# Optimization experiments

Hardware: AMD Instinct MI355X
Metric: run time of the kernel (lower is better)

Reference implementation:

```python
import jax, jax.numpy as jnp
import numpy as np

IN_FEATURES = 1024
OUT_FEATURES = 1024
BATCH = 32768
EPS = 1e-6


def setup_inputs() -> dict:
    key = jax.random.key(0)
    kx, kw = jax.random.split(key)
    x = jax.random.normal(kx, (BATCH, IN_FEATURES), dtype=jnp.float32)
    # xavier-uniform-like init for weight [out, in]
    limit = np.sqrt(6.0 / (IN_FEATURES + OUT_FEATURES)).astype(np.float32)
    W = jax.random.uniform(kw, (OUT_FEATURES, IN_FEATURES), dtype=jnp.float32,
                           minval=-limit, maxval=limit)
    b = jnp.zeros((OUT_FEATURES,), dtype=jnp.float32)
    return {"x": x, "W": W, "b": b}


def reference(x, W, b):
    # sign with sign(0) -> +1
    binary_w = jnp.where(W >= 0, 1.0, -1.0).astype(W.dtype)  # [out, in]
    # per-output-row scale, detached in the original (no grad flows through it)
    scale = jnp.maximum(jnp.mean(jnp.abs(W), axis=1, keepdims=True), EPS)  # [out, 1]
    # F.linear(x, binary_w * scale, b) = x @ (binary_w * scale).T + b
    return jnp.einsum('ni,oi->no', x, binary_w * scale) + b
```

## Files before the change

### kernel.cpp

```cpp
#include <hip/hip_runtime.h>


typedef short short8 __attribute__((ext_vector_type(8)));
typedef float f32x4 __attribute__((ext_vector_type(4)));

#define BATCH 32768
#define IN_F  1024
#define OUT_F 1024
#define EPS   1e-6f

#define BM 128
#define BN 128
#define BK 32

__device__ __forceinline__ ushort f2bf(float f) {
  unsigned u = __builtin_bit_cast(unsigned, f);
  u += 0x7FFFu + ((u >> 16) & 1u);
  return (ushort)(u >> 16);
}

__global__ void bin_kernel(const float* __restrict__ W,
                           ushort* __restrict__ Wb,
                           float* __restrict__ scale) {
  int row = blockIdx.x;
  int t = threadIdx.x;
  const float4* wr = (const float4*)(W + (size_t)row * IN_F);
  ushort4* wb = (ushort4*)(Wb + (size_t)row * IN_F);
  float s = 0.f;
#pragma unroll
  for (int i = 0; i < 4; ++i) {
    float4 v = wr[i * 64 + t];
    ushort4 u;
    u.x = (v.x >= 0.f) ? 0x3F80 : 0xBF80;
    u.y = (v.y >= 0.f) ? 0x3F80 : 0xBF80;
    u.z = (v.z >= 0.f) ? 0x3F80 : 0xBF80;
    u.w = (v.w >= 0.f) ? 0x3F80 : 0xBF80;
    wb[i * 64 + t] = u;
    s += fabsf(v.x) + fabsf(v.y) + fabsf(v.z) + fabsf(v.w);
  }
#pragma unroll
  for (int o = 32; o > 0; o >>= 1) s += __shfl_down(s, o);
  if (t == 0) scale[row] = fmaxf(s * (1.0f / (float)IN_F), EPS);
}

__global__ void gemm_kernel(const float* __restrict__ X,
                            const ushort* __restrict__ Wb,
                            const float* __restrict__ scale,
                            const float* __restrict__ bias,
                            float* __restrict__ out) {
  __shared__ __align__(16) ushort lA[BM * BK];
  __shared__ __align__(16) ushort lB[BN * BK];

  int bid = blockIdx.x;
  int g = (bid & 7) * 256 + (bid >> 3);
  int mt = g >> 3;
  int nt = g & 7;
  int rowBase = mt * BM;
  int colBase = nt * BN;

  int t = threadIdx.x;
  int lane = t & 63;
  int wave = t >> 6;
  int wr = wave >> 1;
  int wc = wave & 1;

  f32x4 acc[4][4];
#pragma unroll
  for (int m = 0; m < 4; ++m)
#pragma unroll
    for (int n = 0; n < 4; ++n) acc[m][n] = (f32x4){0.f, 0.f, 0.f, 0.f};

  for (int kk = 0; kk < IN_F / BK; ++kk) {
    int k0 = kk * BK;
    __syncthreads();

#pragma unroll
    for (int i = 0; i < 2; ++i) {
      int idx = t + 256 * i;
      int r = idx >> 2, c16 = idx & 3;
      const float4* gp =
          (const float4*)(X + (size_t)(rowBase + r) * IN_F + k0 + c16 * 8);
      float4 v0 = gp[0];
      float4 v1 = gp[1];
      short8 u;
      u[0] = (short)f2bf(v0.x); u[1] = (short)f2bf(v0.y);
      u[2] = (short)f2bf(v0.z); u[3] = (short)f2bf(v0.w);
      u[4] = (short)f2bf(v1.x); u[5] = (short)f2bf(v1.y);
      u[6] = (short)f2bf(v1.z); u[7] = (short)f2bf(v1.w);
      int off = (r * BK + c16 * 8) ^ ((r & 7) << 3);
      *(short8*)(&lA[off]) = u;
    }
#pragma unroll
    for (int i = 0; i < 2; ++i) {
      int idx = t + 256 * i;
      int r = idx >> 2, c16 = idx & 3;
      const short8* gp =
          (const short8*)(Wb + (size_t)(colBase + r) * IN_F + k0 + c16 * 8);
      short8 u = *gp;
      int off = (r * BK + c16 * 8) ^ ((r & 7) << 3);
      *(short8*)(&lB[off]) = u;
    }
    __syncthreads();

    short8 af[4], bfr[4];
#pragma unroll
    for (int m = 0; m < 4; ++m) {
      int r = wr * 64 + m * 16 + (lane & 15);
      int off = (r * BK + (lane >> 4) * 8) ^ ((r & 7) << 3);
      af[m] = *(const short8*)(&lA[off]);
    }
#pragma unroll
    for (int n = 0; n < 4; ++n) {
      int r = wc * 64 + n * 16 + (lane & 15);
      int off = (r * BK + (lane >> 4) * 8) ^ ((r & 7) << 3);
      bfr[n] = *(const short8*)(&lB[off]);
    }
#pragma unroll
    for (int m = 0; m < 4; ++m)
#pragma unroll
      for (int n = 0; n < 4; ++n)
        acc[m][n] = __builtin_amdgcn_mfma_f32_16x16x32_bf16(
            af[m], bfr[n], acc[m][n], 0, 0, 0);
  }

#pragma unroll
  for (int n = 0; n < 4; ++n) {
    int col = colBase + wc * 64 + n * 16 + (lane & 15);
    float sc = scale[col];
    float bs = bias[col];
#pragma unroll
    for (int m = 0; m < 4; ++m) {
      int r0 = rowBase + wr * 64 + m * 16 + ((lane >> 4) << 2);
#pragma unroll
      for (int j = 0; j < 4; ++j) {
        out[(size_t)(r0 + j) * OUT_F + col] = acc[m][n][j] * sc + bs;
      }
    }
  }
}

extern "C" void kernel_launch(void* const* d_in, const int* in_sizes, int n_in,
                              void* d_out, int out_size, void* d_ws,
                              size_t ws_size, hipStream_t stream) {
  const float* x = (const float*)d_in[0];
  const float* W = (const float*)d_in[1];
  const float* b = (const float*)d_in[2];
  float* out = (float*)d_out;

  float* scale = (float*)d_ws;
  ushort* Wb = (ushort*)((char*)d_ws + 4096);

  bin_kernel<<<OUT_F, 64, 0, stream>>>(W, Wb, scale);

  dim3 grid((BATCH / BM) * (OUT_F / BN));
  gemm_kernel<<<grid, 256, 0, stream>>>(x, Wb, scale, b, out);
}
```

Baseline: 352.0 us.

## Pre-convert X to bf16 and stage tiles via direct global-to-LDS loads

Adds a separate pass that converts the fp32 activations to bf16 in workspace, then a new GEMM that uses direct global-to-LDS loads with a BK of 64, and falls back to the old kernel when the workspace is too small. The binarize kernel now packs four rows per block. The goal is to halve the bytes the GEMM reads per tile and drop the per-tile fp32-to-bf16 conversion, at the cost of an extra full pass over X (read 128MB, write 64MB). The new LDS layout has no XOR swizzle, which risks bank conflicts on fragment reads.

Measured after the change: 302.6 us. 1.16x faster.

```diff
diff --git a/kernel.cpp b/kernel.cpp
--- a/kernel.cpp
+++ b/kernel.cpp
@@ -11,7 +11,6 @@
 
 #define BM 128
 #define BN 128
-#define BK 32
 
 __device__ __forceinline__ ushort f2bf(float f) {
   unsigned u = __builtin_bit_cast(unsigned, f);
@@ -19,11 +18,17 @@
   return (ushort)(u >> 16);
 }
 
+__device__ __forceinline__ void gload_lds16(const void* g, void* l) {
+  __builtin_amdgcn_global_load_lds(
+      (const __attribute__((address_space(1))) unsigned*)g,
+      (__attribute__((address_space(3))) unsigned*)l, 16, 0, 0);
+}
+
 __global__ void bin_kernel(const float* __restrict__ W,
                            ushort* __restrict__ Wb,
                            float* __restrict__ scale) {
-  int row = blockIdx.x;
-  int t = threadIdx.x;
+  int row = blockIdx.x * 4 + (threadIdx.x >> 6);
+  int t = threadIdx.x & 63;
   const float4* wr = (const float4*)(W + (size_t)row * IN_F);
   ushort4* wb = (ushort4*)(Wb + (size_t)row * IN_F);
   float s = 0.f;
@@ -43,13 +48,22 @@
   if (t == 0) scale[row] = fmaxf(s * (1.0f / (float)IN_F), EPS);
 }
 
-__global__ void gemm_kernel(const float* __restrict__ X,
-                            const ushort* __restrict__ Wb,
-                            const float* __restrict__ scale,
-                            const float* __restrict__ bias,
-                            float* __restrict__ out) {
-  __shared__ __align__(16) ushort lA[BM * BK];
-  __shared__ __align__(16) ushort lB[BN * BK];
+__global__ void cvt_kernel(const float* __restrict__ X,
+                           ushort* __restrict__ Xb) {
+  size_t idx = (size_t)blockIdx.x * 256 + threadIdx.x;
+  float4 v = ((const float4*)X)[idx];
+  ushort4 u;
+  u.x = f2bf(v.x); u.y = f2bf(v.y); u.z = f2bf(v.z); u.w = f2bf(v.w);
+  ((ushort4*)Xb)[idx] = u;
+}
+
+__global__ void gemm_fast(const ushort* __restrict__ Xb,
+                          const ushort* __restrict__ Wb,
+                          const float* __restrict__ scale,
+                          const float* __restrict__ bias,
+                          float* __restrict__ out) {
+  __shared__ __align__(16) ushort lA[BM * 64];
+  __shared__ __align__(16) ushort lB[BN * 64];
 
   int bid = blockIdx.x;
   int g = (bid & 7) * 256 + (bid >> 3);
@@ -64,16 +78,101 @@
   int wr = wave >> 1;
   int wc = wave & 1;
 
+  int srow = (lane >> 3);
+  int scol = (lane & 7) * 8;
+  const ushort* gA = Xb + (size_t)(rowBase + wave * 8 + srow) * IN_F + scol;
+  const ushort* gB = Wb + (size_t)(colBase + wave * 8 + srow) * IN_F + scol;
+  ushort* lA_base = &lA[(wave * 8) * 64];
+  ushort* lB_base = &lB[(wave * 8) * 64];
+
   f32x4 acc[4][4];
 #pragma unroll
   for (int m = 0; m < 4; ++m)
 #pragma unroll
     for (int n = 0; n < 4; ++n) acc[m][n] = (f32x4){0.f, 0.f, 0.f, 0.f};
 
-  for (int kk = 0; kk < IN_F / BK; ++kk) {
-    int k0 = kk * BK;
-    __syncthreads();
-
+  for (int kk = 0; kk < IN_F / 64; ++kk) {
+    int k0 = kk * 64;
+    __syncthreads();
+
+#pragma unroll
+    for (int j = 0; j < 4; ++j) {
+      gload_lds16(gA + k0 + (size_t)j * 32 * IN_F, lA_base + j * 32 * 64);
+      gload_lds16(gB + k0 + (size_t)j * 32 * IN_F, lB_base + j * 32 * 64);
+    }
+    __syncthreads();
+
+    short8 af[4][2], bfx[4][2];
+#pragma unroll
+    for (int m = 0; m < 4; ++m)
+#pragma unroll
+      for (int ks = 0; ks < 2; ++ks) {
+        int row = wr * 64 + m * 16 + (lane & 15);
+        af[m][ks] = *(const short8*)(&lA[row * 64 + ks * 32 + (lane >> 4) * 8]);
+      }
+#pragma unroll
+    for (int n = 0; n < 4; ++n)
+#pragma unroll
+      for (int ks = 0; ks < 2; ++ks) {
+        int row = wc * 64 + n * 16 + (lane & 15);
+        bfx[n][ks] = *(const short8*)(&lB[row * 64 + ks * 32 + (lane >> 4) * 8]);
+      }
+#pragma unroll
+    for (int ks = 0; ks < 2; ++ks)
+#pragma unroll
+      for (int m = 0; m < 4; ++m)
+#pragma unroll
+        for (int n = 0; n < 4; ++n)
+          acc[m][n] = __builtin_amdgcn_mfma_f32_16x16x32_bf16(
+              af[m][ks], bfx[n][ks], acc[m][n], 0, 0, 0);
+  }
+
+#pragma unroll
+  for (int n = 0; n < 4; ++n) {
+    int col = colBase + wc * 64 + n * 16 + (lane & 15);
+    float sc = scale[col];
+    float bs = bias[col];
+#pragma unroll
+    for (int m = 0; m < 4; ++m) {
+      int r0 = rowBase + wr * 64 + m * 16 + ((lane >> 4) << 2);
+#pragma unroll
+      for (int j = 0; j < 4; ++j) {
+        out[(size_t)(r0 + j) * OUT_F + col] = acc[m][n][j] * sc + bs;
+      }
+    }
+  }
+}
+
+__global__ void gemm_kernel(const float* __restrict__ X,
+                            const ushort* __restrict__ Wb,
+                            const float* __restrict__ scale,
+                            const float* __restrict__ bias,
+                            float* __restrict__ out) {
+  __shared__ __align__(16) ushort lA[BM * 32];
+  __shared__ __align__(16) ushort lB[BN * 32];
+
+  int bid = blockIdx.x;
+  int g = (bid & 7) * 256 + (bid >> 3);
+  int mt = g >> 3;
+  int nt = g & 7;
+  int rowBase = mt * BM;
+  int colBase = nt * BN;
+
+  int t = threadIdx.x;
+  int lane = t & 63;
+  int wave = t >> 6;
+  int wr = wave >> 1;
+  int wc = wave & 1;
+
+  f32x4 acc[4][4];
+#pragma unroll
+  for (int m = 0; m < 4; ++m)
+#pragma unroll
+    for (int n = 0; n < 4; ++n) acc[m][n] = (f32x4){0.f, 0.f, 0.f, 0.f};
+
+  for (int kk = 0; kk < IN_F / 32; ++kk) {
+    int k0 = kk * 32;
+    __syncthreads();
 #pragma unroll
     for (int i = 0; i < 2; ++i) {
       int idx = t + 256 * i;
@@ -87,7 +186,7 @@
       u[2] = (short)f2bf(v0.z); u[3] = (short)f2bf(v0.w);
       u[4] = (short)f2bf(v1.x); u[5] = (short)f2bf(v1.y);
       u[6] = (short)f2bf(v1.z); u[7] = (short)f2bf(v1.w);
-      int off = (r * BK + c16 * 8) ^ ((r & 7) << 3);
+      int off = (r * 32 + c16 * 8) ^ ((r & 7) << 3);
       *(short8*)(&lA[off]) = u;
     }
 #pragma unroll
@@ -97,7 +196,7 @@
       const short8* gp =
           (const short8*)(Wb + (size_t)(colBase + r) * IN_F + k0 + c16 * 8);
       short8 u = *gp;
-      int off = (r * BK + c16 * 8) ^ ((r & 7) << 3);
+      int off = (r * 32 + c16 * 8) ^ ((r & 7) << 3);
       *(short8*)(&lB[off]) = u;
     }
     __syncthreads();
@@ -106,13 +205,13 @@
 #pragma unroll
     for (int m = 0; m < 4; ++m) {
       int r = wr * 64 + m * 16 + (lane & 15);
-      int off = (r * BK + (lane >> 4) * 8) ^ ((r & 7) << 3);
+      int off = (r * 32 + (lane >> 4) * 8) ^ ((r & 7) << 3);
       af[m] = *(const short8*)(&lA[off]);
     }
 #pragma unroll
     for (int n = 0; n < 4; ++n) {
       int r = wc * 64 + n * 16 + (lane & 15);
-      int off = (r * BK + (lane >> 4) * 8) ^ ((r & 7) << 3);
+      int off = (r * 32 + (lane >> 4) * 8) ^ ((r & 7) << 3);
       bfr[n] = *(const short8*)(&lB[off]);
     }
 #pragma unroll
@@ -149,9 +248,16 @@
 
   float* scale = (float*)d_ws;
   ushort* Wb = (ushort*)((char*)d_ws + 4096);
-
-  bin_kernel<<<OUT_F, 64, 0, stream>>>(W, Wb, scale);
+  ushort* xb = (ushort*)((char*)d_ws + 4096 + 2097152);
+  const size_t need = 4096 + 2097152 + (size_t)BATCH * IN_F * 2;
+
+  bin_kernel<<<OUT_F / 4, 256, 0, stream>>>(W, Wb, scale);
 
   dim3 grid((BATCH / BM) * (OUT_F / BN));
-  gemm_kernel<<<grid, 256, 0, stream>>>(x, Wb, scale, b, out);
-}
+  if (ws_size >= need) {
+    cvt_kernel<<<(BATCH * IN_F / 4) / 256, 256, 0, stream>>>(x, xb);
+    gemm_fast<<<grid, 256, 0, stream>>>(xb, Wb, scale, b, out);
+  } else {
+    gemm_kernel<<<grid, 256, 0, stream>>>(x, Wb, scale, b, out);
+  }
+}
```
